# Kernel optimization log

Hardware: AMD Instinct MI355X
Metric: run time of the kernel (lower is better)

The kernel has to match this reference:

```python
import jax, jax.numpy as jnp
import numpy as np

BETA_THRESH = 0.1   # threshold fraction in forward and cos_batch
TWD_WEIGHT = 0.1    # args.twd_weight
IPOT_BETA = 0.5     # default beta in IPOT_torch_batch_uniform
EPS_MASK = 1e-05


def _cos_cost(x, y):
    # x: (b, d, n), y: (b, d, m) -> 1 - cosine similarity, shape (b, n, m)
    xn = x / (jnp.linalg.norm(x, axis=1, keepdims=True) + 1e-12)
    yn = y / (jnp.linalg.norm(y, axis=1, keepdims=True) + 1e-12)
    return 1.0 - jnp.einsum('bdn,bdm->bnm', xn, yn)


def _threshold_relu(c):
    # global (over whole batch) min/max threshold, as in torch .min()/.max()
    mn, mx = c.min(), c.max()
    thr = mn + BETA_THRESH * (mx - mn)
    return jax.nn.relu(c - thr)


def _ipot(C, n, m, iters):
    # IPOT proximal point iteration with uniform marginals. C: (b, n, m)
    bs = C.shape[0]
    A = jnp.exp(-C / IPOT_BETA)
    T0 = jnp.ones((bs, n, m), C.dtype)
    s0 = jnp.full((bs, m, 1), 1.0 / m, C.dtype)

    def body(carry, _):
        T, sigma = carry
        Q = A * T                                             # (b, n, m)
        delta = 1.0 / (n * jnp.matmul(Q, sigma))              # (b, n, 1)
        sigma = 1.0 / (m * jnp.matmul(jnp.swapaxes(Q, 1, 2), delta))  # (b, m, 1)
        T = delta * Q * jnp.swapaxes(sigma, 1, 2)
        return (T, sigma), None

    (T, _), _ = jax.lax.scan(body, (T0, s0), None, length=iters)
    return T


def _ipot_distance(C, n, m, iters):
    T = _ipot(C, n, m, iters)
    # batch_trace(C^T @ T) == sum(C * T) per batch, kept as (b, 1)
    dist = jnp.einsum('bnm,bnm->b', C, T)[:, None]
    return -dist, T


def _gw_distance_uniform(X, Y, token_dep_mask, image_rel_mask, iteration, ot_iteration):
    # X: (b, d, n_img), Y: (b, d, n_tok); masks weight the intra-modal graphs
    bs, _, n = X.shape
    m = Y.shape[2]
    p = jnp.full((bs, n, 1), 1.0 / n, X.dtype)
    q = jnp.full((bs, m, 1), 1.0 / m, X.dtype)
    Cs = _threshold_relu(_cos_cost(X, X)) * image_rel_mask    # (b, n, n)
    Ct = _threshold_relu(_cos_cost(Y, Y)) * token_dep_mask    # (b, m, m)
    # Cst = (Cs^2 p) 1_m^T + 1_n (q^T (Ct^2)^T), via broadcasting
    Cst = jnp.matmul(Cs ** 2, p) + jnp.swapaxes(jnp.matmul(Ct ** 2, q), 1, 2)  # (b, n, m)
    gamma = jnp.matmul(p, jnp.swapaxes(q, 1, 2))              # (b, n, m)
    for _ in range(iteration):
        C_gamma = Cst - 2.0 * jnp.einsum('bnk,bkl,bml->bnm', Cs, gamma, Ct)
        gamma = _ipot(C_gamma, n, m, ot_iteration)
    C_gamma = Cst - 2.0 * jnp.einsum('bnk,bkl,bml->bnm', Cs, gamma, Ct)
    T = jax.lax.stop_gradient(gamma)  # gamma.detach() in torch
    dist = jnp.einsum('bnm,bnm->b', C_gamma, T)[:, None]
    return dist, T


def setup_inputs() -> dict:
    key = jax.random.key(0)
    k1, k2, k3, k4 = jax.random.split(key, 4)
    bs, n_img, n_tok, d = 32, 196, 256, 1024
    return {
        'image_feature': jax.random.normal(k1, (bs, n_img, d), jnp.float32),
        'token_feature': jax.random.normal(k2, (bs, n_tok, d), jnp.float32),
        'token_mask': jnp.ones((bs, n_tok), jnp.float32),
        'token_dependency_masks': jax.random.randint(k3, (bs, n_tok, n_tok), 0, 2, jnp.int32),
        'image_rel_mask': jax.random.randint(k4, (bs, n_img, n_img), 0, 2, jnp.int32),
    }


def reference(image_feature, token_feature, token_mask, token_dependency_masks, image_rel_mask):
    dt = image_feature.dtype
    token_feature = token_feature * token_mask[:, :, None]
    img_t = jnp.swapaxes(image_feature, 1, 2)  # (b, d, n)
    tok_t = jnp.swapaxes(token_feature, 1, 2)  # (b, d, m)
    # cost_matrix_batch_torch returns (b, m, n); forward transposes back to (b, n, m)
    cos_distance = _cos_cost(img_t, tok_t)     # (b, n, m)
    irm = jnp.where(image_rel_mask == 1, 1.0, EPS_MASK).astype(dt)
    tdm = jnp.where(token_dependency_masks == 1, 1.0, EPS_MASK).astype(dt)
    cos_dist = _threshold_relu(cos_distance)
    n = image_feature.shape[1]
    m = token_feature.shape[1]
    wd, T_wd = _ipot_distance(cos_dist, n, m, 20)
    gwd, T_gwd = _gw_distance_uniform(img_t, tok_t, tdm, irm, iteration=5, ot_iteration=20)
    twd = TWD_WEIGHT * jnp.mean(gwd) + TWD_WEIGHT * jnp.mean(wd)
    return twd, T_wd, T_gwd
```

## Files before the change

kernel.cpp:

```cpp
#include <hip/hip_runtime.h>
#include <math.h>

#define BS 32
#define NI 196
#define NT 256
#define DD 1024

typedef unsigned int u32;
typedef __attribute__((ext_vector_type(8))) short bf16x8;
typedef __attribute__((ext_vector_type(4))) float f32x4;

__device__ __forceinline__ u32 fenc(float f){ u32 u = __float_as_uint(f); return (u & 0x80000000u) ? ~u : (u | 0x80000000u); }
__device__ __forceinline__ float fdec(u32 u){ return __uint_as_float((u & 0x80000000u) ? (u & 0x7fffffffu) : ~u); }

__device__ __forceinline__ unsigned short f2bf(float f){
  u32 u = __float_as_uint(f);
  u32 r = (u + 0x7FFFu + ((u >> 16) & 1u)) >> 16;
  return (unsigned short)r;
}
__device__ __forceinline__ float bf2f(unsigned short h){ return __uint_as_float((u32)h << 16); }

template<int CTRL>
__device__ __forceinline__ float dppadd(float x){
  int y = __builtin_amdgcn_update_dpp(0, __float_as_int(x), CTRL, 0xF, 0xF, false);
  return x + __int_as_float(y);
}
__device__ __forceinline__ float rowsum32(float x){
  x = dppadd<0xB1>(x);
  x = dppadd<0x4E>(x);
  x = dppadd<0x141>(x);
  x = dppadd<0x128>(x);
  x += __shfl_xor(x, 16);
  return x;
}

__global__ void init_mm_k(u32* mm){
  int t = threadIdx.x;
  if (t < 3){ mm[2*t] = 0xFFFFFFFFu; mm[2*t+1] = 0u; }
}

__global__ __launch_bounds__(256) void prep_k(const float* __restrict__ feat,
                                              const float* __restrict__ mask,
                                              unsigned short* __restrict__ hi,
                                              unsigned short* __restrict__ lo, int R){
  int b = blockIdx.y, r = blockIdx.x, t = threadIdx.x;
  size_t rowoff = ((size_t)b*R + r)*DD;
  float4 v = ((const float4*)(feat + rowoff))[t];
  float s = v.x*v.x + v.y*v.y + v.z*v.z + v.w*v.w;
  #pragma unroll
  for (int m = 32; m >= 1; m >>= 1) s += __shfl_xor(s, m);
  __shared__ float ps[4];
  if ((t & 63) == 0) ps[t >> 6] = s;
  __syncthreads();
  float tot = ps[0] + ps[1] + ps[2] + ps[3];
  float mv = mask ? mask[b*R + r] : 1.0f;
  float sc = mv / (mv * sqrtf(tot) + 1e-12f);
  float x[4] = {v.x*sc, v.y*sc, v.z*sc, v.w*sc};
  unsigned short h[4], l[4];
  #pragma unroll
  for (int i = 0; i < 4; ++i){
    h[i] = f2bf(x[i]);
    l[i] = f2bf(x[i] - bf2f(h[i]));
  }
  *(ushort4*)(hi + rowoff + t*4) = make_ushort4(h[0],h[1],h[2],h[3]);
  *(ushort4*)(lo + rowoff + t*4) = make_ushort4(l[0],l[1],l[2],l[3]);
}

__global__ __launch_bounds__(256) void cosmm_k(const unsigned short* __restrict__ Xh,
                                               const unsigned short* __restrict__ Xl,
                                               const unsigned short* __restrict__ Yh,
                                               const unsigned short* __restrict__ Yl,
                                               float* __restrict__ C, int M, int N, int nTN){
  __shared__ unsigned short Ah[128*40], Al[128*40], Bh[128*40], Bl[128*40];
  int b = blockIdx.y;
  int tm = (blockIdx.x / nTN) * 128, tn = (blockIdx.x % nTN) * 128;
  int t = threadIdx.x, lane = t & 63, w = t >> 6;
  int wm = (w >> 1) * 64, wn = (w & 1) * 64;
  const unsigned short* Xhb = Xh + (size_t)b*M*DD;
  const unsigned short* Xlb = Xl + (size_t)b*M*DD;
  const unsigned short* Yhb = Yh + (size_t)b*N*DD;
  const unsigned short* Ylb = Yl + (size_t)b*N*DD;
  f32x4 acc[4][4];
  #pragma unroll
  for (int m = 0; m < 4; ++m)
    #pragma unroll
    for (int n = 0; n < 4; ++n) acc[m][n] = (f32x4){0.f,0.f,0.f,0.f};

  int sr0 = t >> 2, sc0 = (t & 3) * 8;
  int gr0 = min(tm + sr0, M-1),      gr1 = min(tm + sr0 + 64, M-1);
  int gc0 = min(tn + sr0, N-1),      gc1 = min(tn + sr0 + 64, N-1);
  const unsigned short* pa0 = Xhb + (size_t)gr0*DD + sc0;
  const unsigned short* pa1 = Xhb + (size_t)gr1*DD + sc0;
  const unsigned short* pa2 = Xlb + (size_t)gr0*DD + sc0;
  const unsigned short* pa3 = Xlb + (size_t)gr1*DD + sc0;
  const unsigned short* pb0 = Yhb + (size_t)gc0*DD + sc0;
  const unsigned short* pb1 = Yhb + (size_t)gc1*DD + sc0;
  const unsigned short* pb2 = Ylb + (size_t)gc0*DD + sc0;
  const unsigned short* pb3 = Ylb + (size_t)gc1*DD + sc0;
  int fr = lane & 15, fk = (lane >> 4) * 8;

  for (int k0 = 0; k0 < DD; k0 += 32){
    float4 a0 = *(const float4*)(pa0 + k0);
    float4 a1 = *(const float4*)(pa1 + k0);
    float4 a2 = *(const float4*)(pa2 + k0);
    float4 a3 = *(const float4*)(pa3 + k0);
    float4 b0 = *(const float4*)(pb0 + k0);
    float4 b1 = *(const float4*)(pb1 + k0);
    float4 b2 = *(const float4*)(pb2 + k0);
    float4 b3 = *(const float4*)(pb3 + k0);
    __syncthreads();
    *(float4*)&Ah[sr0*40 + sc0]      = a0;
    *(float4*)&Ah[(sr0+64)*40 + sc0] = a1;
    *(float4*)&Al[sr0*40 + sc0]      = a2;
    *(float4*)&Al[(sr0+64)*40 + sc0] = a3;
    *(float4*)&Bh[sr0*40 + sc0]      = b0;
    *(float4*)&Bh[(sr0+64)*40 + sc0] = b1;
    *(float4*)&Bl[sr0*40 + sc0]      = b2;
    *(float4*)&Bl[(sr0+64)*40 + sc0] = b3;
    __syncthreads();
    bf16x8 ah[4], al[4], bh[4], bl[4];
    #pragma unroll
    for (int m = 0; m < 4; ++m){
      int r = wm + m*16 + fr;
      ah[m] = *(bf16x8*)&Ah[r*40 + fk];
      al[m] = *(bf16x8*)&Al[r*40 + fk];
    }
    #pragma unroll
    for (int n = 0; n < 4; ++n){
      int r = wn + n*16 + fr;
      bh[n] = *(bf16x8*)&Bh[r*40 + fk];
      bl[n] = *(bf16x8*)&Bl[r*40 + fk];
    }
    #pragma unroll
    for (int m = 0; m < 4; ++m)
      #pragma unroll
      for (int n = 0; n < 4; ++n){
        acc[m][n] = __builtin_amdgcn_mfma_f32_16x16x32_bf16(ah[m], bh[n], acc[m][n], 0,0,0);
        acc[m][n] = __builtin_amdgcn_mfma_f32_16x16x32_bf16(ah[m], bl[n], acc[m][n], 0,0,0);
        acc[m][n] = __builtin_amdgcn_mfma_f32_16x16x32_bf16(al[m], bh[n], acc[m][n], 0,0,0);
      }
  }
  float* Cb = C + (size_t)b*M*N;
  #pragma unroll
  for (int m = 0; m < 4; ++m){
    int row0 = tm + wm + m*16 + ((lane >> 4) << 2);
    #pragma unroll
    for (int n = 0; n < 4; ++n){
      int col = tn + wn + n*16 + (lane & 15);
      if (col < N){
        #pragma unroll
        for (int r = 0; r < 4; ++r){
          int row = row0 + r;
          if (row < M) Cb[(size_t)row*N + col] = 1.0f - acc[m][n][r];
        }
      }
    }
  }
}

template<int EPI>
__global__ __launch_bounds__(256) void mmnt_k(const unsigned short* __restrict__ Ah,
                                              const unsigned short* __restrict__ Al,
                                              const unsigned short* __restrict__ Bh,
                                              const unsigned short* __restrict__ Bl,
                                              float* __restrict__ C,
                                              int M, int N, int Kp, int nTN,
                                              const float* __restrict__ av,
                                              const float* __restrict__ bv){
  __shared__ unsigned short As_h[64*40], As_l[64*40], Bs_h[64*40], Bs_l[64*40];
  int b = blockIdx.y;
  int tm = (blockIdx.x / nTN) * 64, tn = (blockIdx.x % nTN) * 64;
  int t = threadIdx.x, lane = t & 63, w = t >> 6;
  int wm = (w >> 1) * 32, wn = (w & 1) * 32;
  const unsigned short* Ahb = Ah + (size_t)b*M*Kp;
  const unsigned short* Alb = Al + (size_t)b*M*Kp;
  const unsigned short* Bhb = Bh + (size_t)b*N*Kp;
  const unsigned short* Blb = Bl + (size_t)b*N*Kp;
  f32x4 acc[2][2];
  #pragma unroll
  for (int m = 0; m < 2; ++m)
    #pragma unroll
    for (int n = 0; n < 2; ++n) acc[m][n] = (f32x4){0.f,0.f,0.f,0.f};

  int srow = t >> 2, sch = (t & 3) * 8;
  int ga = min(tm + srow, M-1), gbn = min(tn + srow, N-1);
  const unsigned short* pah = Ahb + (size_t)ga*Kp + sch;
  const unsigned short* pal = Alb + (size_t)ga*Kp + sch;
  const unsigned short* pbh = Bhb + (size_t)gbn*Kp + sch;
  const unsigned short* pbl = Blb + (size_t)gbn*Kp + sch;
  int fr = lane & 15, fk = (lane >> 4) * 8;

  for (int k0 = 0; k0 < Kp; k0 += 32){
    float4 vah = *(const float4*)(pah + k0);
    float4 val = *(const float4*)(pal + k0);
    float4 vbh = *(const float4*)(pbh + k0);
    float4 vbl = *(const float4*)(pbl + k0);
    __syncthreads();
    *(float4*)&As_h[srow*40 + sch] = vah;
    *(float4*)&As_l[srow*40 + sch] = val;
    *(float4*)&Bs_h[srow*40 + sch] = vbh;
    *(float4*)&Bs_l[srow*40 + sch] = vbl;
    __syncthreads();
    bf16x8 fah[2], fal[2], fbh[2], fbl[2];
    #pragma unroll
    for (int m = 0; m < 2; ++m){
      int r = wm + m*16 + fr;
      fah[m] = *(bf16x8*)&As_h[r*40 + fk];
      fal[m] = *(bf16x8*)&As_l[r*40 + fk];
    }
    #pragma unroll
    for (int n = 0; n < 2; ++n){
      int r = wn + n*16 + fr;
      fbh[n] = *(bf16x8*)&Bs_h[r*40 + fk];
      fbl[n] = *(bf16x8*)&Bs_l[r*40 + fk];
    }
    #pragma unroll
    for (int m = 0; m < 2; ++m)
      #pragma unroll
      for (int n = 0; n < 2; ++n){
        acc[m][n] = __builtin_amdgcn_mfma_f32_16x16x32_bf16(fah[m], fbh[n], acc[m][n], 0,0,0);
        acc[m][n] = __builtin_amdgcn_mfma_f32_16x16x32_bf16(fah[m], fbl[n], acc[m][n], 0,0,0);
        acc[m][n] = __builtin_amdgcn_mfma_f32_16x16x32_bf16(fal[m], fbh[n], acc[m][n], 0,0,0);
      }
  }
  float* Cb = C + (size_t)b*M*N;
  #pragma unroll
  for (int m = 0; m < 2; ++m){
    int row0 = tm + wm + m*16 + ((lane >> 4) << 2);
    #pragma unroll
    for (int n = 0; n < 2; ++n){
      int col = tn + wn + n*16 + (lane & 15);
      #pragma unroll
      for (int r = 0; r < 4; ++r){
        int row = row0 + r;
        if (row < M){
          float x = acc[m][n][r];
          if (EPI == 2) x = av[b*M + row] + bv[b*N + col] - 2.0f*x;
          Cb[(size_t)row*N + col] = x;
        }
      }
    }
  }
}

__global__ __launch_bounds__(256) void split_k(const float* __restrict__ src,
                                               unsigned short* __restrict__ dsth,
                                               unsigned short* __restrict__ dstl,
                                               int Cin, int Kp){
  int r = blockIdx.x, b = blockIdx.y, j = threadIdx.x, R = gridDim.x;
  if (j >= Kp) return;
  float v = (j < Cin) ? src[((size_t)b*R + r)*Cin + j] : 0.f;
  unsigned short h = f2bf(v);
  unsigned short l = f2bf(v - bf2f(h));
  size_t o = ((size_t)b*R + r)*Kp + j;
  dsth[o] = h; dstl[o] = l;
}

__global__ __launch_bounds__(256) void splitT_k(const float* __restrict__ g,
                                                unsigned short* __restrict__ th,
                                                unsigned short* __restrict__ tl){
  __shared__ float tile[32][33];
  int j0 = blockIdx.x * 32, k0 = blockIdx.y * 32, b = blockIdx.z;
  int t = threadIdx.x;
  const float* gb = g + (size_t)b*NI*NT;
  {
    int a = t >> 3, ch = t & 7;
    int k = k0 + a;
    float4 v = make_float4(0.f,0.f,0.f,0.f);
    if (k < NI) v = *(const float4*)(gb + (size_t)k*NT + j0 + ch*4);
    tile[a][ch*4+0] = v.x; tile[a][ch*4+1] = v.y; tile[a][ch*4+2] = v.z; tile[a][ch*4+3] = v.w;
  }
  __syncthreads();
  {
    int jloc = t >> 3, ch = t & 7;
    int j = j0 + jloc;
    unsigned short h[4], l[4];
    #pragma unroll
    for (int r = 0; r < 4; ++r){
      float v = tile[ch*4 + r][jloc];
      h[r] = f2bf(v);
      l[r] = f2bf(v - bf2f(h[r]));
    }
    size_t o = ((size_t)b*NT + j)*224 + k0 + ch*4;
    *(ushort4*)(th + o) = make_ushort4(h[0],h[1],h[2],h[3]);
    *(ushort4*)(tl + o) = make_ushort4(l[0],l[1],l[2],l[3]);
  }
}

__global__ __launch_bounds__(256) void minmax_k(const float* __restrict__ X, size_t cnt, u32* __restrict__ mm){
  size_t stride = (size_t)gridDim.x * blockDim.x;
  float mn = 3.402823466e38f, mx = -3.402823466e38f;
  for (size_t i = (size_t)blockIdx.x*blockDim.x + threadIdx.x; i < cnt; i += stride){
    float v = X[i]; mn = fminf(mn, v); mx = fmaxf(mx, v);
  }
  #pragma unroll
  for (int m = 32; m >= 1; m >>= 1){ mn = fminf(mn, __shfl_xor(mn, m)); mx = fmaxf(mx, __shfl_xor(mx, m)); }
  __shared__ float smn[4], smx[4];
  int t = threadIdx.x;
  if ((t & 63) == 0){ smn[t>>6] = mn; smx[t>>6] = mx; }
  __syncthreads();
  if (t == 0){
    mn = fminf(fminf(smn[0], smn[1]), fminf(smn[2], smn[3]));
    mx = fmaxf(fmaxf(smx[0], smx[1]), fmaxf(smx[2], smx[3]));
    atomicMin(&mm[0], fenc(mn));
    atomicMax(&mm[1], fenc(mx));
  }
}

__global__ __launch_bounds__(256) void thresh_k(float* __restrict__ X, const int* __restrict__ msk,
                                                size_t cnt, const u32* __restrict__ mm){
  float mn = fdec(mm[0]), mx = fdec(mm[1]);
  float thr = mn + 0.1f * (mx - mn);
  size_t stride = (size_t)gridDim.x * blockDim.x;
  for (size_t i = (size_t)blockIdx.x*blockDim.x + threadIdx.x; i < cnt; i += stride){
    float v = X[i] - thr;
    v = v > 0.f ? v : 0.f;
    if (msk) v *= (msk[i] == 1 ? 1.0f : 1e-5f);
    X[i] = v;
  }
}

__global__ __launch_bounds__(64) void rowmeansq_k(const float* __restrict__ X, float* __restrict__ out, int R, int Cc){
  int b = blockIdx.y, r = blockIdx.x, t = threadIdx.x;
  const float* row = X + ((size_t)b*R + r) * Cc;
  float s = 0.f;
  for (int j = t; j < Cc; j += 64){ float v = row[j]; s = fmaf(v, v, s); }
  #pragma unroll
  for (int m = 32; m >= 1; m >>= 1) s += __shfl_xor(s, m);
  if (t == 0) out[b*R + r] = s / (float)Cc;
}

__global__ void fill_k(float* __restrict__ X, size_t cnt, float val){
  size_t stride = (size_t)gridDim.x * blockDim.x;
  for (size_t i = (size_t)blockIdx.x*blockDim.x + threadIdx.x; i < cnt; i += stride) X[i] = val;
}

template<bool WD>
__global__ __launch_bounds__(512, 2) void ipotr_k(const float* __restrict__ Cmat,
                                                  float* __restrict__ Tout,
                                                  float* __restrict__ distBuf){
  __shared__ float cp[16][NT];
  __shared__ float sgm[NT];
  __shared__ float wp[8];
  int b = blockIdx.x, t = threadIdx.x;
  int c = t & 31, R = t >> 5;
  const float* Cb = Cmat + (size_t)b * NI * NT;
  bool ok12 = (R < 4);
  float Cv[13][8], T[13][8];
  #pragma unroll
  for (int k = 0; k < 13; ++k){
    int i = R + 16*k;
    bool ok = (k < 12) | ok12;
    #pragma unroll
    for (int l = 0; l < 8; ++l){
      Cv[k][l] = ok ? Cb[(size_t)i*NT + c + 32*l] : 1.0e3f;
      T[k][l]  = ok ? 1.f : 0.f;
    }
  }
  float sl[8];
  #pragma unroll
  for (int l = 0; l < 8; ++l) sl[l] = 1.0f / (float)NT;

  for (int it = 0; it < 20; ++it){
    float cpl[8];
    #pragma unroll
    for (int l = 0; l < 8; ++l) cpl[l] = 0.f;
    #pragma unroll
    for (int k = 0; k < 13; ++k){
      float a = 0.f;
      #pragma unroll
      for (int l = 0; l < 8; ++l){
        float q = __expf(-2.0f * Cv[k][l]) * T[k][l];
        T[k][l] = q;
        a = fmaf(q, sl[l], a);
      }
      a = rowsum32(a);
      float dl = __builtin_amdgcn_rcpf((float)NI * a);
      if (k == 12) dl = ok12 ? dl : 0.f;
      #pragma unroll
      for (int l = 0; l < 8; ++l){
        T[k][l] *= dl;
        cpl[l] += T[k][l];
      }
    }
    #pragma unroll
    for (int l = 0; l < 8; ++l) cp[R][c + 32*l] = cpl[l];
    __syncthreads();
    if (t < NT){
      float s = 0.f;
      #pragma unroll
      for (int g = 0; g < 16; ++g) s += cp[g][t];
      sgm[t] = __builtin_amdgcn_rcpf((float)NT * s);
    }
    __syncthreads();
    #pragma unroll
    for (int l = 0; l < 8; ++l) sl[l] = sgm[c + 32*l];
    #pragma unroll
    for (int k = 0; k < 13; ++k)
      #pragma unroll
      for (int l = 0; l < 8; ++l) T[k][l] *= sl[l];
  }
  float* To = Tout + (size_t)b * NI * NT;
  #pragma unroll
  for (int k = 0; k < 13; ++k){
    int i = R + 16*k;
    if ((k < 12) | ok12){
      #pragma unroll
      for (int l = 0; l < 8; ++l) To[(size_t)i*NT + c + 32*l] = T[k][l];
    }
  }
  if (WD){
    float a = 0.f;
    #pragma unroll
    for (int k = 0; k < 13; ++k)
      #pragma unroll
      for (int l = 0; l < 8; ++l) a = fmaf(Cv[k][l] < 5.0e2f ? Cv[k][l] : 0.f, T[k][l], a);
    #pragma unroll
    for (int m = 32; m >= 1; m >>= 1) a += __shfl_xor(a, m);
    if ((t & 63) == 0) wp[t >> 6] = a;
    __syncthreads();
    if (t == 0){
      float s = 0.f;
      #pragma unroll
      for (int g = 0; g < 8; ++g) s += wp[g];
      distBuf[b] = -s;
    }
  }
}

__global__ __launch_bounds__(256) void gwdist_k(const float* __restrict__ Cg, const float* __restrict__ gam,
                                                float* __restrict__ outT, float* __restrict__ gwd){
  int b = blockIdx.x, t = threadIdx.x;
  const float* cb = Cg + (size_t)b*NI*NT;
  const float* gb = gam + (size_t)b*NI*NT;
  float* ob = outT + (size_t)b*NI*NT;
  float a = 0.f;
  for (int i = t; i < NI*NT; i += 256){
    float g = gb[i];
    a = fmaf(cb[i], g, a);
    ob[i] = g;
  }
  #pragma unroll
  for (int m = 32; m >= 1; m >>= 1) a += __shfl_xor(a, m);
  __shared__ float ps[4];
  if ((t & 63) == 0) ps[t>>6] = a;
  __syncthreads();
  if (t == 0) gwd[b] = ps[0]+ps[1]+ps[2]+ps[3];
}

__global__ void fin_k(const float* __restrict__ wd, const float* __restrict__ gwd, float* __restrict__ out){
  int t = threadIdx.x;
  float w = (t < BS) ? wd[t] : 0.f;
  float g = (t < BS) ? gwd[t] : 0.f;
  #pragma unroll
  for (int m = 32; m >= 1; m >>= 1){ w += __shfl_xor(w, m); g += __shfl_xor(g, m); }
  if (t == 0) out[0] = 0.1f * (g / (float)BS) + 0.1f * (w / (float)BS);
}

extern "C" void kernel_launch(void* const* d_in, const int* in_sizes, int n_in,
                              void* d_out, int out_size, void* d_ws, size_t ws_size,
                              hipStream_t stream){
  const float* img  = (const float*)d_in[0];
  const float* tok  = (const float*)d_in[1];
  const float* tmsk = (const float*)d_in[2];
  const int*   tdm  = (const int*)d_in[3];
  const int*   irm  = (const int*)d_in[4];
  float* out = (float*)d_out;

  float* ws = (float*)d_ws;
  size_t off = 0;
  float* cosIT = ws + off; off += (size_t)BS*NI*NT;
  float* Cs    = ws + off; off += (size_t)BS*NI*NI;
  float* Ct    = ws + off; off += (size_t)BS*NT*NT;
  float* Xreg  = ws + off; off += (size_t)BS*NI*DD;
  float* gamma = Xreg;
  float* Cgam  = Xreg + (size_t)BS*NI*NT;
  float* G1    = Xreg + (size_t)2*BS*NI*NT;
  unsigned short* Xh = (unsigned short*)Xreg;
  unsigned short* Xl = Xh + (size_t)BS*NI*DD;
  float* Yreg  = ws + off; off += (size_t)BS*NT*DD;
  unsigned short* Yh = (unsigned short*)Yreg;
  unsigned short* Yl = Yh + (size_t)BS*NT*DD;
  {
  }
  unsigned short* Csh = (unsigned short*)Yreg;
  unsigned short* Csl = Csh + (size_t)BS*NI*224;
  unsigned short* Cth = Csl + (size_t)BS*NI*224;
  unsigned short* Ctl = Cth + (size_t)BS*NT*256;
  unsigned short* gTh = Ctl + (size_t)BS*NT*256;
  unsigned short* gTl = gTh + (size_t)BS*NT*224;
  unsigned short* G1h = gTl + (size_t)BS*NT*224;
  unsigned short* G1l = G1h + (size_t)BS*NI*256;
  float* avec  = ws + off; off += (size_t)BS*NI;
  float* bvec  = ws + off; off += (size_t)BS*NT;
  u32*   mm    = (u32*)(ws + off); off += 8;
  float* wd_b  = ws + off; off += BS;
  float* gwd_b = ws + off; off += BS;

  init_mm_k<<<1, 64, 0, stream>>>(mm);

  prep_k<<<dim3(NI,BS), 256, 0, stream>>>(img, nullptr, Xh, Xl, NI);
  prep_k<<<dim3(NT,BS), 256, 0, stream>>>(tok, tmsk,    Yh, Yl, NT);

  cosmm_k<<<dim3(4, BS), 256, 0, stream>>>(Xh, Xl, Yh, Yl, cosIT, NI, NT, 2);
  cosmm_k<<<dim3(4, BS), 256, 0, stream>>>(Xh, Xl, Xh, Xl, Cs,    NI, NI, 2);
  cosmm_k<<<dim3(4, BS), 256, 0, stream>>>(Yh, Yl, Yh, Yl, Ct,    NT, NT, 2);

  minmax_k<<<512, 256, 0, stream>>>(cosIT, (size_t)BS*NI*NT, mm+0);
  minmax_k<<<512, 256, 0, stream>>>(Cs,    (size_t)BS*NI*NI, mm+2);
  minmax_k<<<512, 256, 0, stream>>>(Ct,    (size_t)BS*NT*NT, mm+4);
  thresh_k<<<1024, 256, 0, stream>>>(cosIT, nullptr, (size_t)BS*NI*NT, mm+0);
  thresh_k<<<1024, 256, 0, stream>>>(Cs,    irm,     (size_t)BS*NI*NI, mm+2);
  thresh_k<<<1024, 256, 0, stream>>>(Ct,    tdm,     (size_t)BS*NT*NT, mm+4);

  rowmeansq_k<<<dim3(NI,BS), 64, 0, stream>>>(Cs, avec, NI, NI);
  rowmeansq_k<<<dim3(NT,BS), 64, 0, stream>>>(Ct, bvec, NT, NT);

  split_k<<<dim3(NI,BS), 256, 0, stream>>>(Cs, Csh, Csl, NI, 224);
  split_k<<<dim3(NT,BS), 256, 0, stream>>>(Ct, Cth, Ctl, NT, 256);

  ipotr_k<true><<<BS, 512, 0, stream>>>(cosIT, out + 1, wd_b);

  fill_k<<<512, 256, 0, stream>>>(gamma, (size_t)BS*NI*NT, 1.0f/((float)NI*(float)NT));
  for (int itn = 0; itn < 6; ++itn){
    splitT_k<<<dim3(8, 7, BS), 256, 0, stream>>>(gamma, gTh, gTl);
    mmnt_k<0><<<dim3(16, BS), 256, 0, stream>>>(Csh, Csl, gTh, gTl, G1, NI, NT, 224, 4, nullptr, nullptr);
    split_k<<<dim3(NI,BS), 256, 0, stream>>>(G1, G1h, G1l, NT, 256);
    mmnt_k<2><<<dim3(16, BS), 256, 0, stream>>>(G1h, G1l, Cth, Ctl, Cgam, NI, NT, 256, 4, avec, bvec);
    if (itn < 5)
      ipotr_k<false><<<BS, 512, 0, stream>>>(Cgam, gamma, nullptr);
  }

  gwdist_k<<<BS, 256, 0, stream>>>(Cgam, gamma, out + 1 + (size_t)BS*NI*NT, gwd_b);
  fin_k<<<1, 64, 0, stream>>>(wd_b, gwd_b, out);
}
```

Before: 996.6 us.

## Precompute exp kernel once into LDS as bf16 and halve IPOT block size

```diff
diff --git a/kernel.cpp b/kernel.cpp
--- a/kernel.cpp
+++ b/kernel.cpp
@@ -336,47 +336,69 @@
 }
 
 template<bool WD>
-__global__ __launch_bounds__(512, 2) void ipotr_k(const float* __restrict__ Cmat,
-                                                  float* __restrict__ Tout,
-                                                  float* __restrict__ distBuf){
-  __shared__ float cp[16][NT];
+__global__ __launch_bounds__(256, 1) void ipotr3_k(const float* __restrict__ Cmat,
+                                                   float* __restrict__ Tout,
+                                                   float* __restrict__ distBuf){
+  __shared__ u32 Ppk[8*25*32*4];
+  __shared__ float cp[8][NT];
   __shared__ float sgm[NT];
-  __shared__ float wp[8];
+  __shared__ float wp[4];
+  const u32 HIM = 0xFFFF0000u;
   int b = blockIdx.x, t = threadIdx.x;
   int c = t & 31, R = t >> 5;
   const float* Cb = Cmat + (size_t)b * NI * NT;
-  bool ok12 = (R < 4);
-  float Cv[13][8], T[13][8];
-  #pragma unroll
-  for (int k = 0; k < 13; ++k){
-    int i = R + 16*k;
-    bool ok = (k < 12) | ok12;
-    #pragma unroll
-    for (int l = 0; l < 8; ++l){
-      Cv[k][l] = ok ? Cb[(size_t)i*NT + c + 32*l] : 1.0e3f;
-      T[k][l]  = ok ? 1.f : 0.f;
-    }
-  }
+  bool ok24 = (R < 4);
+  u32* myP = &Ppk[((R*25)*32 + c)*4];
+
+  float T[25][8];
+  #pragma unroll
+  for (int k = 0; k < 25; ++k){
+    int i = R + 8*k;
+    bool ok = (k < 24) | ok24;
+    float cv[8];
+    #pragma unroll
+    for (int l = 0; l < 8; ++l)
+      cv[l] = ok ? Cb[(size_t)i*NT + c + 32*l] : 0.f;
+    u32 pk[4];
+    #pragma unroll
+    for (int j = 0; j < 4; ++j){
+      float p0 = ok ? __expf(-2.0f*cv[2*j])   : 0.f;
+      float p1 = ok ? __expf(-2.0f*cv[2*j+1]) : 0.f;
+      pk[j] = (u32)f2bf(p0) | ((u32)f2bf(p1) << 16);
+    }
+    *(uint4*)(myP + k*128) = make_uint4(pk[0], pk[1], pk[2], pk[3]);
+    #pragma unroll
+    for (int l = 0; l < 8; ++l) T[k][l] = ok ? 1.f : 0.f;
+  }
+
   float sl[8];
   #pragma unroll
   for (int l = 0; l < 8; ++l) sl[l] = 1.0f / (float)NT;
 
+  #pragma unroll 1
   for (int it = 0; it < 20; ++it){
     float cpl[8];
     #pragma unroll
     for (int l = 0; l < 8; ++l) cpl[l] = 0.f;
     #pragma unroll
-    for (int k = 0; k < 13; ++k){
+    for (int k = 0; k < 25; ++k){
+      uint4 pq = *(const uint4*)(myP + k*128);
+      u32 ps[4] = {pq.x, pq.y, pq.z, pq.w};
       float a = 0.f;
       #pragma unroll
-      for (int l = 0; l < 8; ++l){
-        float q = __expf(-2.0f * Cv[k][l]) * T[k][l];
-        T[k][l] = q;
-        a = fmaf(q, sl[l], a);
+      for (int j = 0; j < 4; ++j){
+        float pe = __uint_as_float(ps[j] << 16);
+        float po = __uint_as_float(ps[j] & HIM);
+        float qe = pe * T[k][2*j];
+        float qo = po * T[k][2*j+1];
+        T[k][2*j]   = qe;
+        T[k][2*j+1] = qo;
+        a = fmaf(qe, sl[2*j], a);
+        a = fmaf(qo, sl[2*j+1], a);
       }
       a = rowsum32(a);
       float dl = __builtin_amdgcn_rcpf((float)NI * a);
-      if (k == 12) dl = ok12 ? dl : 0.f;
+      if (k == 24) dl = ok24 ? dl : 0.f;
       #pragma unroll
       for (int l = 0; l < 8; ++l){
         T[k][l] *= dl;
@@ -386,45 +408,40 @@
     #pragma unroll
     for (int l = 0; l < 8; ++l) cp[R][c + 32*l] = cpl[l];
     __syncthreads();
-    if (t < NT){
+    {
       float s = 0.f;
       #pragma unroll
-      for (int g = 0; g < 16; ++g) s += cp[g][t];
+      for (int g = 0; g < 8; ++g) s += cp[g][t];
       sgm[t] = __builtin_amdgcn_rcpf((float)NT * s);
     }
     __syncthreads();
     #pragma unroll
     for (int l = 0; l < 8; ++l) sl[l] = sgm[c + 32*l];
     #pragma unroll
-    for (int k = 0; k < 13; ++k)
+    for (int k = 0; k < 25; ++k)
       #pragma unroll
       for (int l = 0; l < 8; ++l) T[k][l] *= sl[l];
   }
+
   float* To = Tout + (size_t)b * NI * NT;
-  #pragma unroll
-  for (int k = 0; k < 13; ++k){
-    int i = R + 16*k;
-    if ((k < 12) | ok12){
-      #pragma unroll
-      for (int l = 0; l < 8; ++l) To[(size_t)i*NT + c + 32*l] = T[k][l];
+  float acc = 0.f;
+  #pragma unroll
+  for (int k = 0; k < 25; ++k){
+    int i = R + 8*k;
+    if ((k < 24) | ok24){
+      #pragma unroll
+      for (int l = 0; l < 8; ++l){
+        To[(size_t)i*NT + c + 32*l] = T[k][l];
+        if (WD) acc = fmaf(Cb[(size_t)i*NT + c + 32*l], T[k][l], acc);
+      }
     }
   }
   if (WD){
-    float a = 0.f;
-    #pragma unroll
-    for (int k = 0; k < 13; ++k)
-      #pragma unroll
-      for (int l = 0; l < 8; ++l) a = fmaf(Cv[k][l] < 5.0e2f ? Cv[k][l] : 0.f, T[k][l], a);
-    #pragma unroll
-    for (int m = 32; m >= 1; m >>= 1) a += __shfl_xor(a, m);
-    if ((t & 63) == 0) wp[t >> 6] = a;
-    __syncthreads();
-    if (t == 0){
-      float s = 0.f;
-      #pragma unroll
-      for (int g = 0; g < 8; ++g) s += wp[g];
-      distBuf[b] = -s;
-    }
+    #pragma unroll
+    for (int m = 32; m >= 1; m >>= 1) acc += __shfl_xor(acc, m);
+    if ((t & 63) == 0) wp[t >> 6] = acc;
+    __syncthreads();
+    if (t == 0) distBuf[b] = -(wp[0] + wp[1] + wp[2] + wp[3]);
   }
 }
 
@@ -481,8 +498,6 @@
   float* Yreg  = ws + off; off += (size_t)BS*NT*DD;
   unsigned short* Yh = (unsigned short*)Yreg;
   unsigned short* Yl = Yh + (size_t)BS*NT*DD;
-  {
-  }
   unsigned short* Csh = (unsigned short*)Yreg;
   unsigned short* Csl = Csh + (size_t)BS*NI*224;
   unsigned short* Cth = Csl + (size_t)BS*NI*224;
@@ -519,7 +534,7 @@
   split_k<<<dim3(NI,BS), 256, 0, stream>>>(Cs, Csh, Csl, NI, 224);
   split_k<<<dim3(NT,BS), 256, 0, stream>>>(Ct, Cth, Ctl, NT, 256);
 
-  ipotr_k<true><<<BS, 512, 0, stream>>>(cosIT, out + 1, wd_b);
+  ipotr3_k<true><<<BS, 256, 0, stream>>>(cosIT, out + 1, wd_b);
 
   fill_k<<<512, 256, 0, stream>>>(gamma, (size_t)BS*NI*NT, 1.0f/((float)NI*(float)NT));
   for (int itn = 0; itn < 6; ++itn){
@@ -528,7 +543,7 @@
     split_k<<<dim3(NI,BS), 256, 0, stream>>>(G1, G1h, G1l, NT, 256);
     mmnt_k<2><<<dim3(16, BS), 256, 0, stream>>>(G1h, G1l, Cth, Ctl, Cgam, NI, NT, 256, 4, avec, bvec);
     if (itn < 5)
-      ipotr_k<false><<<BS, 512, 0, stream>>>(Cgam, gamma, nullptr);
+      ipotr3_k<false><<<BS, 256, 0, stream>>>(Cgam, gamma, nullptr);
   }
 
   gwdist_k<<<BS, 256, 0, stream>>>(Cgam, gamma, out + 1 + (size_t)BS*NI*NT, gwd_b);
```

Result: slower. 1.158 ms (+16.2%).
